# Performance work log

Hardware: AMD Instinct MI355X
Metric: run time of the kernel (lower is better)

The kernel has to match this reference:

```python
import jax, jax.numpy as jnp
import numpy as np

# Hardware-emulation constants (from init_kwargs, NeuroSim-style QLinear)
WL_IN = 8        # input activation bit width (bit-serial)
WL_W = 8         # weight bit width
CELL_BIT = 2     # bits per memory cell -> 4 weight slices
SUB = 128        # crossbar sub-array size (rows summed in analog)
ADC_BITS = 5     # ADC precision per partial sum
ONOFF = 10.0     # cell on/off conductance ratio
VARI = 0.05      # multiplicative device variation sigma


def _adc_quant(x, bits, axes):
    # LinearQuantizeOut: uniform quantization between tensor min/max
    mn = jnp.min(x, axis=axes, keepdims=True)
    mx = jnp.max(x, axis=axes, keepdims=True)
    step = (mx - mn) * (2.0 ** (-bits))
    step = jnp.where(step <= 0, 1.0, step)
    idx = jnp.clip(jnp.floor((x - mn) / step), 0.0, 2.0 ** bits - 1.0)
    return idx * step + mn


def _qlinear_hw(x, w, noise):
    """Analog PIM crossbar emulation of y = x @ w.T with bit-serial inputs,
    bit-sliced cells, on/off-ratio offset + dummy column, device variation,
    per-subarray ADC quantization."""
    B, N = x.shape
    F = w.shape[0]
    I, W, K = WL_IN, WL_W, WL_W // CELL_BIT
    cr = 2.0 ** CELL_BIT
    lower, upper = 1.0 / ONOFF, 1.0
    S = (N + SUB - 1) // SUB
    Np = S * SUB
    # quantize input to I bits in [0,1]; weight to W-bit integer in [0, 2^W-1]
    xq = jnp.round(jnp.clip(x, 0.0, 1.0) * (2.0 ** I - 1.0))            # [B, N]
    Xi = jnp.clip(jnp.round((w + 1.0) * 0.5 * (2.0 ** W - 1.0)), 0.0, 2.0 ** W - 1.0)  # [F, N]
    xq = jnp.pad(xq, ((0, 0), (0, Np - N)))
    Xi = jnp.pad(Xi, ((0, 0), (0, Np - N)))
    zpow = 2.0 ** jnp.arange(I, dtype=x.dtype)
    kpow = cr ** jnp.arange(K, dtype=x.dtype)
    bits = jnp.mod(jnp.floor(xq[..., None] / zpow), 2.0)                # [B, Np, I]
    slc = jnp.mod(jnp.floor(Xi[..., None] / kpow), cr)                  # [F, Np, K]
    g = slc * (upper - lower) + (cr - 1.0) * lower                      # cell conductances
    g = g * (1.0 + VARI * noise)                                        # device variation
    bits = bits.reshape(B, S, SUB, I)
    g = g.reshape(F, S, SUB, K)
    # analog partial sums per (input bit i, subarray s, weight slice k)
    P = jnp.einsum('bsai,fsak->iskbf', bits, g)                         # [I,S,K,B,F]
    # dummy column (all cells at lowest conductance), identical across F
    D = jnp.transpose(bits.sum(axis=2), (2, 1, 0)) * ((cr - 1.0) * lower)  # [I,S,B]
    Pq = _adc_quant(P, ADC_BITS, axes=(3, 4))
    Dq = _adc_quant(D, ADC_BITS, axes=(2,))
    scal = (2.0 ** jnp.arange(I, dtype=x.dtype))[:, None] * (cr ** jnp.arange(K, dtype=x.dtype))[None, :]
    acc = jnp.einsum('iskbf,ik->bf', Pq - Dq[:, :, None, :, None], scal) / (upper - lower)
    # undo integer mappings: w = 2*Xi/(2^W-1) - 1, x = xq/(2^I-1)
    out = 2.0 * acc / ((2.0 ** I - 1.0) * (2.0 ** W - 1.0)) \
          - xq.sum(axis=1, keepdims=True) / (2.0 ** I - 1.0)
    return out


def _qlinear(x, w, noise):
    # straight-through quantized weight (WAGE-style STE) + hardware forward
    Xi = jnp.clip(jnp.round((w + 1.0) * 0.5 * (2.0 ** WL_W - 1.0)), 0.0, 2.0 ** WL_W - 1.0)
    wq = 2.0 * Xi / (2.0 ** WL_W - 1.0) - 1.0
    wq_ste = w + jax.lax.stop_gradient(wq - w)
    out_ideal = x @ wq_ste.T
    out_hw = _qlinear_hw(x, w, noise)
    return out_ideal + jax.lax.stop_gradient(out_hw - out_ideal)


def setup_inputs() -> dict:
    key = jax.random.key(0)
    k1, k2, k3, k4, k5 = jax.random.split(key, 5)
    x = jax.random.uniform(k1, (1024, 784), dtype=jnp.float32)
    w1 = jax.random.normal(k2, (512, 784), dtype=jnp.float32) * 0.05
    w3 = jax.random.normal(k3, (10, 512), dtype=jnp.float32) * 0.08
    noise1 = jax.random.normal(k4, (512, 896, 4), dtype=jnp.float32)  # 784 padded to 7*128
    noise3 = jax.random.normal(k5, (10, 512, 4), dtype=jnp.float32)   # 512 = 4*128 exact
    return {"x": x, "w1": w1, "w3": w3, "noise1": noise1, "noise3": noise3}


def reference(x, w1, w3, noise1, noise3):
    h = jnp.tanh(_qlinear(x, w1, noise1))   # QLinear(784,512) + Tanh
    return _qlinear(h, w3, noise3)          # QLinear(512,10)
```

## Files before the change

### kernel.cpp

```cpp
#include <hip/hip_runtime.h>

#define FLTMAX 3.402823466e+38f


__global__ void init_kernel(float* __restrict__ acc1, unsigned* __restrict__ stats1)
{
    int gid = blockIdx.x * 256 + threadIdx.x;
    if (gid < 1024 * 512) acc1[gid] = 0.f;
    if (gid < 224) { stats1[gid * 2] = 0x7F7FFFFFu; stats1[gid * 2 + 1] = 0u; }
}

__global__ void prep1_kernel(const float* __restrict__ x, float* __restrict__ xq1,
                             float* __restrict__ sx1)
{
    __shared__ float red[128];
    int b = blockIdx.x;
    float psum = 0.f;
    for (int n = threadIdx.x; n < 896; n += 128) {
        float v = 0.f;
        if (n < 784) {
            float xv = x[b * 784 + n];
            xv = fminf(fmaxf(xv, 0.f), 1.f);
            v = rintf(__fmul_rn(xv, 255.f));
        }
        xq1[b * 896 + n] = v;
        psum += v;
    }
    red[threadIdx.x] = psum;
    __syncthreads();
    for (int w = 64; w >= 1; w >>= 1) {
        if (threadIdx.x < w) red[threadIdx.x] += red[threadIdx.x + w];
        __syncthreads();
    }
    if (threadIdx.x == 0) sx1[b] = red[0];
}

__global__ void prepg1_kernel(const float* __restrict__ w1, const float* __restrict__ noise1,
                              float* __restrict__ g1)
{
    int gid = blockIdx.x * 256 + threadIdx.x;
    if (gid >= 512 * 896) return;
    int f = gid / 896, n = gid % 896;
    float gv[4] = {0.f, 0.f, 0.f, 0.f};
    if (n < 784) {
        float w = w1[f * 784 + n];
        float Xi = fminf(fmaxf(rintf(__fmul_rn(__fmul_rn(__fadd_rn(w, 1.f), 0.5f), 255.f)),
                               0.f), 255.f);
        int xi = (int)Xi;
#pragma unroll
        for (int k = 0; k < 4; ++k) {
            int slc = (xi >> (2 * k)) & 3;
            float base = __fadd_rn(__fmul_rn((float)slc, 0.9f), 0.3f);
            float nf = __fadd_rn(1.f, __fmul_rn(0.05f, noise1[(f * 896 + n) * 4 + k]));
            gv[k] = __fmul_rn(base, nf);
        }
    }
#pragma unroll
    for (int k = 0; k < 4; ++k) g1[(k * 512 + f) * 896 + n] = gv[k];
}

__global__ void transpose_kernel(const float* __restrict__ in, float* __restrict__ out,
                                 int R, int C)
{
    __shared__ float tile[32][33];
    int c0 = blockIdx.x * 32, r0 = blockIdx.y * 32;
    int tx = threadIdx.x & 31, ty4 = (threadIdx.x >> 5) * 4;
#pragma unroll
    for (int u = 0; u < 4; ++u)
        tile[ty4 + u][tx] = in[(r0 + ty4 + u) * C + c0 + tx];
    __syncthreads();
#pragma unroll
    for (int u = 0; u < 4; ++u)
        out[(c0 + ty4 + u) * R + r0 + tx] = tile[tx][ty4 + u];
}

__global__ void prepg2_kernel(const float* __restrict__ w3, const float* __restrict__ noise3,
                              float* __restrict__ g2t)
{
    int gid = blockIdx.x * 256 + threadIdx.x;
    if (gid >= 10 * 512) return;
    int f = gid / 512, n = gid % 512;
    float w = w3[f * 512 + n];
    float Xi = fminf(fmaxf(rintf(__fmul_rn(__fmul_rn(__fadd_rn(w, 1.f), 0.5f), 255.f)),
                           0.f), 255.f);
    int xi = (int)Xi;
#pragma unroll
    for (int k = 0; k < 4; ++k) {
        int slc = (xi >> (2 * k)) & 3;
        float base = __fadd_rn(__fmul_rn((float)slc, 0.9f), 0.3f);
        float nf = __fadd_rn(1.f, __fmul_rn(0.05f, noise3[(f * 512 + n) * 4 + k]));
        g2t[n * 40 + k * 10 + f] = __fmul_rn(base, nf);
    }
}

__global__ void dq_kernel(const float* __restrict__ xq, float* __restrict__ Dq,
                          int S, int rowstride)
{
    __shared__ float red[512];
    const int i = blockIdx.x / S, s = blockIdx.x % S;
    const int tid = threadIdx.x;
    float D[4];
    float mn = FLTMAX, mx = -FLTMAX;
#pragma unroll
    for (int u = 0; u < 4; ++u) {
        int b = tid + u * 256;
        const float4* row = (const float4*)&xq[b * rowstride + s * 128];
        int c = 0;
#pragma unroll 8
        for (int q = 0; q < 32; ++q) {
            float4 v = row[q];
            c += (((int)v.x >> i) & 1) + (((int)v.y >> i) & 1) +
                 (((int)v.z >> i) & 1) + (((int)v.w >> i) & 1);
        }
        D[u] = __fmul_rn((float)c, 0.3f);
        mn = fminf(mn, D[u]);
        mx = fmaxf(mx, D[u]);
    }
    red[tid] = mn; red[256 + tid] = mx;
    __syncthreads();
    for (int w = 128; w >= 1; w >>= 1) {
        if (tid < w) {
            red[tid] = fminf(red[tid], red[tid + w]);
            red[256 + tid] = fmaxf(red[256 + tid], red[256 + tid + w]);
        }
        __syncthreads();
    }
    mn = red[0]; mx = red[256];
    float step = __fmul_rn(__fsub_rn(mx, mn), 0.03125f);
    if (step <= 0.f) step = 1.f;
#pragma unroll
    for (int u = 0; u < 4; ++u) {
        int b = tid + u * 256;
        float idx = fminf(fmaxf(floorf(__fdiv_rn(__fsub_rn(D[u], mn), step)), 0.f), 31.f);
        Dq[(i * S + s) * 1024 + b] = __fadd_rn(__fmul_rn(idx, step), mn);
    }
}

__global__ void dterm_kernel(const float* __restrict__ Dq, float* __restrict__ dterm, int S)
{
    int b = blockIdx.x * 256 + threadIdx.x;
    if (b >= 1024) return;
    float sum = 0.f;
    for (int i = 0; i < 8; ++i) {
        float sc = (float)(85 << i);
        for (int s = 0; s < S; ++s) sum = fmaf(Dq[(i * S + s) * 1024 + b], sc, sum);
    }
    dterm[b] = sum;
}

#define BK 32
__global__ __launch_bounds__(256, 4) void mm1_kernel(
    const float* __restrict__ xqT, const float* __restrict__ g1t,
    float* __restrict__ P, unsigned* __restrict__ stats, int s, int i0)
{
    __shared__ __align__(16) float As[BK][132];
    __shared__ __align__(16) float Bs[BK][132];
    __shared__ float red[512];
    const int tid = threadIdx.x;
    const int rowChunk = blockIdx.x * 128;
    const int i = i0 + (rowChunk >> 10);
    const int b0 = rowChunk & 1023;
    const int colBase = blockIdx.y * 128;
    const int nbase = s * 128;
    const int tx = tid & 15, ty = tid >> 4;

    float acc[8][8] = {};
    for (int ac = 0; ac < 4; ++ac) {
        const int n0 = nbase + ac * BK;
        __syncthreads();
#pragma unroll
        for (int u = 0; u < 4; ++u) {
            int t = u * 256 + tid;
            int a = t >> 5;
            int e = (t & 31) << 2;
            float4 av = *(const float4*)&xqT[(n0 + a) * 1024 + b0 + e];
            float4 bv = *(const float4*)&g1t[(n0 + a) * 2048 + colBase + e];
            float4 ab;
            ab.x = (float)((((int)av.x) >> i) & 1);
            ab.y = (float)((((int)av.y) >> i) & 1);
            ab.z = (float)((((int)av.z) >> i) & 1);
            ab.w = (float)((((int)av.w) >> i) & 1);
            *(float4*)&As[a][e] = ab;
            *(float4*)&Bs[a][e] = bv;
        }
        __syncthreads();
#pragma unroll 4
        for (int a = 0; a < BK; ++a) {
            float ar[8], br[8];
            *(float4*)&ar[0] = *(const float4*)&As[a][ty << 2];
            *(float4*)&ar[4] = *(const float4*)&As[a][64 + (ty << 2)];
            *(float4*)&br[0] = *(const float4*)&Bs[a][tx << 2];
            *(float4*)&br[4] = *(const float4*)&Bs[a][64 + (tx << 2)];
#pragma unroll
            for (int u = 0; u < 8; ++u)
#pragma unroll
                for (int v = 0; v < 8; ++v)
                    acc[u][v] = fmaf(ar[u], br[v], acc[u][v]);
        }
    }

#pragma unroll
    for (int uh = 0; uh < 2; ++uh)
#pragma unroll
        for (int u = 0; u < 4; ++u) {
            int row = rowChunk + uh * 64 + (ty << 2) + u;
#pragma unroll
            for (int vh = 0; vh < 2; ++vh) {
                float4 v = make_float4(acc[uh * 4 + u][vh * 4 + 0], acc[uh * 4 + u][vh * 4 + 1],
                                       acc[uh * 4 + u][vh * 4 + 2], acc[uh * 4 + u][vh * 4 + 3]);
                *(float4*)&P[(size_t)row * 2048 + colBase + vh * 64 + (tx << 2)] = v;
            }
        }

    float mn = acc[0][0], mx = acc[0][0];
#pragma unroll
    for (int u = 0; u < 8; ++u)
#pragma unroll
        for (int v = 0; v < 8; ++v) { mn = fminf(mn, acc[u][v]); mx = fmaxf(mx, acc[u][v]); }
    red[tid] = mn; red[256 + tid] = mx;
    __syncthreads();
    for (int w = 128; w >= 1; w >>= 1) {
        if (tid < w) {
            red[tid] = fminf(red[tid], red[tid + w]);
            red[256 + tid] = fmaxf(red[256 + tid], red[256 + tid + w]);
        }
        __syncthreads();
    }
    if (tid == 0) {
        int k = colBase >> 9;
        int slot = ((s * 8 + i) * 4 + k) * 2;
        atomicMin(&stats[slot], __float_as_uint(red[0]));
        atomicMax(&stats[slot + 1], __float_as_uint(red[256]));
    }
}

__global__ void quant1_kernel(const float* __restrict__ P, const unsigned* __restrict__ stats,
                              float* __restrict__ acc1, int s, int i0, int ni)
{
    int gid = blockIdx.x * 256 + threadIdx.x;
    int b = gid >> 9, f = gid & 511;
    float sum = 0.f;
    for (int il = 0; il < ni; ++il) {
        int i = i0 + il;
#pragma unroll
        for (int k = 0; k < 4; ++k) {
            int slot = ((s * 8 + i) * 4 + k) * 2;
            float mn = __uint_as_float(stats[slot]);
            float mx = __uint_as_float(stats[slot + 1]);
            float step = __fmul_rn(__fsub_rn(mx, mn), 0.03125f);
            if (step <= 0.f) step = 1.f;
            float val = P[(size_t)(il * 1024 + b) * 2048 + (k << 9) + f];
            float idx = fminf(fmaxf(floorf(__fdiv_rn(__fsub_rn(val, mn), step)), 0.f), 31.f);
            float pq = __fadd_rn(__fmul_rn(idx, step), mn);
            sum = fmaf(pq, (float)(1 << (i + 2 * k)), sum);
        }
    }
    acc1[gid] += sum;
}

__global__ void finish1_kernel(const float* __restrict__ acc1, const float* __restrict__ dterm1,
                               const float* __restrict__ sx1, float* __restrict__ xq2)
{
    int gid = blockIdx.x * 256 + threadIdx.x;
    int b = gid >> 9;
    float total = __fsub_rn(acc1[gid], dterm1[b]);
    float acc = __fdiv_rn(total, 0.9f);
    float o = __fsub_rn(__fdiv_rn(__fmul_rn(2.f, acc), 65025.f), __fdiv_rn(sx1[b], 255.f));
    float h = tanhf(o);
    h = fminf(fmaxf(h, 0.f), 1.f);
    xq2[gid] = rintf(__fmul_rn(h, 255.f));
}

__global__ void sx2_kernel(const float* __restrict__ xq2, float* __restrict__ sx2)
{
    __shared__ float red[128];
    int b = blockIdx.x;
    float psum = 0.f;
    for (int n = threadIdx.x; n < 512; n += 128) psum += xq2[b * 512 + n];
    red[threadIdx.x] = psum;
    __syncthreads();
    for (int w = 64; w >= 1; w >>= 1) {
        if (threadIdx.x < w) red[threadIdx.x] += red[threadIdx.x + w];
        __syncthreads();
    }
    if (threadIdx.x == 0) sx2[b] = red[0];
}

__global__ void mm2_kernel(const float* __restrict__ xq2, const float* __restrict__ g2t,
                           float* __restrict__ P2)
{
    int gid = blockIdx.x * 256 + threadIdx.x;
    if (gid >= 40960) return;
    int f = gid % 10;
    int b = (gid / 10) & 1023;
    int s = gid / 10240;
    float acc[8][4] = {};
    for (int a = 0; a < 128; ++a) {
        int n = s * 128 + a;
        int xi = (int)xq2[b * 512 + n];
        float g0 = g2t[n * 40 + f];
        float gA = g2t[n * 40 + 10 + f];
        float gB = g2t[n * 40 + 20 + f];
        float gC = g2t[n * 40 + 30 + f];
#pragma unroll
        for (int i = 0; i < 8; ++i) {
            float bi = (float)((xi >> i) & 1);
            acc[i][0] = fmaf(bi, g0, acc[i][0]);
            acc[i][1] = fmaf(bi, gA, acc[i][1]);
            acc[i][2] = fmaf(bi, gB, acc[i][2]);
            acc[i][3] = fmaf(bi, gC, acc[i][3]);
        }
    }
#pragma unroll
    for (int i = 0; i < 8; ++i)
#pragma unroll
        for (int k = 0; k < 4; ++k)
            P2[(size_t)((s * 8 + i) * 4 + k) * 10240 + b * 10 + f] = acc[i][k];
}

__global__ void stat2_kernel(const float* __restrict__ P2, float2* __restrict__ stats2)
{
    __shared__ float red[512];
    int p = blockIdx.x;
    int tid = threadIdx.x;
    float mn = FLTMAX, mx = -FLTMAX;
    for (int t = tid; t < 10240; t += 256) {
        float v = P2[(size_t)p * 10240 + t];
        mn = fminf(mn, v); mx = fmaxf(mx, v);
    }
    red[tid] = mn; red[256 + tid] = mx;
    __syncthreads();
    for (int w = 128; w >= 1; w >>= 1) {
        if (tid < w) {
            red[tid] = fminf(red[tid], red[tid + w]);
            red[256 + tid] = fmaxf(red[256 + tid], red[256 + tid + w]);
        }
        __syncthreads();
    }
    if (tid == 0) {
        float step = __fmul_rn(__fsub_rn(red[256], red[0]), 0.03125f);
        if (step <= 0.f) step = 1.f;
        stats2[p] = make_float2(red[0], step);
    }
}

__global__ void out2_kernel(const float* __restrict__ P2, const float2* __restrict__ stats2,
                            const float* __restrict__ dterm2, const float* __restrict__ sx2,
                            float* __restrict__ out)
{
    int gid = blockIdx.x * 256 + threadIdx.x;
    if (gid >= 10240) return;
    int b = gid / 10;
    float sum = 0.f;
    for (int s = 0; s < 4; ++s)
        for (int i = 0; i < 8; ++i)
#pragma unroll
            for (int k = 0; k < 4; ++k) {
                int p = (s * 8 + i) * 4 + k;
                float2 st = stats2[p];
                float val = P2[(size_t)p * 10240 + gid];
                float idx = fminf(fmaxf(floorf(__fdiv_rn(__fsub_rn(val, st.x), st.y)), 0.f), 31.f);
                float pq = __fadd_rn(__fmul_rn(idx, st.y), st.x);
                sum = fmaf(pq, (float)(1 << (i + 2 * k)), sum);
            }
    float total = __fsub_rn(sum, dterm2[b]);
    float acc = __fdiv_rn(total, 0.9f);
    out[gid] = __fsub_rn(__fdiv_rn(__fmul_rn(2.f, acc), 65025.f), __fdiv_rn(sx2[b], 255.f));
}

extern "C" void kernel_launch(void* const* d_in, const int* in_sizes, int n_in,
                              void* d_out, int out_size, void* d_ws, size_t ws_size,
                              hipStream_t stream)
{
    const float* x      = (const float*)d_in[0];
    const float* w1     = (const float*)d_in[1];
    const float* w3     = (const float*)d_in[2];
    const float* noise1 = (const float*)d_in[3];
    const float* noise3 = (const float*)d_in[4];
    float* out = (float*)d_out;
    float* ws  = (float*)d_ws;

    float*    xq1    = ws + 0;
    float*    g1     = ws + 917504;
    float*    acc1   = ws + 2752512;
    float*    xq2    = ws + 3276800;
    float*    P2     = ws + 3801088;
    float*    g2t    = ws + 5111808;
    float*    Dq1    = ws + 5132288;
    float*    Dq2    = ws + 5189632;
    float*    sx1    = ws + 5222400;
    float*    sx2    = ws + 5223424;
    float*    dterm1 = ws + 5224448;
    float*    dterm2 = ws + 5225472;
    float2*   stats2 = (float2*)(ws + 5226496);
    unsigned* stats1 = (unsigned*)(ws + 5226752);
    float*    xqT    = ws + 5227200;
    float*    g1t    = ws + 6144704;
    float*    Ps     = ws + 7979712;

    const size_t fixedf = 7979712;
    int ni = 8;
    while (ni > 1 && (fixedf + (size_t)ni * 2097152) * sizeof(float) > ws_size) ni >>= 1;

    init_kernel<<<2048, 256, 0, stream>>>(acc1, stats1);
    prep1_kernel<<<1024, 128, 0, stream>>>(x, xq1, sx1);
    prepg1_kernel<<<1792, 256, 0, stream>>>(w1, noise1, g1);
    transpose_kernel<<<dim3(28, 32), 256, 0, stream>>>(xq1, xqT, 1024, 896);
    transpose_kernel<<<dim3(28, 64), 256, 0, stream>>>(g1, g1t, 2048, 896);
    dq_kernel<<<56, 256, 0, stream>>>(xq1, Dq1, 7, 896);
    dterm_kernel<<<4, 256, 0, stream>>>(Dq1, dterm1, 7);

    for (int s = 0; s < 7; ++s)
        for (int i0 = 0; i0 < 8; i0 += ni) {
            mm1_kernel<<<dim3(8 * ni, 16), 256, 0, stream>>>(xqT, g1t, Ps, stats1, s, i0);
            quant1_kernel<<<2048, 256, 0, stream>>>(Ps, stats1, acc1, s, i0, ni);
        }

    finish1_kernel<<<2048, 256, 0, stream>>>(acc1, dterm1, sx1, xq2);
    sx2_kernel<<<1024, 128, 0, stream>>>(xq2, sx2);
    prepg2_kernel<<<20, 256, 0, stream>>>(w3, noise3, g2t);
    dq_kernel<<<32, 256, 0, stream>>>(xq2, Dq2, 4, 512);
    dterm_kernel<<<4, 256, 0, stream>>>(Dq2, dterm2, 4);
    mm2_kernel<<<160, 256, 0, stream>>>(xq2, g2t, P2);
    stat2_kernel<<<128, 256, 0, stream>>>(P2, stats2);
    out2_kernel<<<40, 256, 0, stream>>>(P2, stats2, dterm2, sx2, out);
}
```

Measured before the change: 683.6 us.

## Enlarge mm1 tile with register prefetch, vectorize quant, fuse g1 prep and transpose

```diff
diff --git a/kernel.cpp b/kernel.cpp
--- a/kernel.cpp
+++ b/kernel.cpp
@@ -35,28 +35,49 @@
     if (threadIdx.x == 0) sx1[b] = red[0];
 }
 
-__global__ void prepg1_kernel(const float* __restrict__ w1, const float* __restrict__ noise1,
-                              float* __restrict__ g1)
-{
-    int gid = blockIdx.x * 256 + threadIdx.x;
-    if (gid >= 512 * 896) return;
-    int f = gid / 896, n = gid % 896;
-    float gv[4] = {0.f, 0.f, 0.f, 0.f};
-    if (n < 784) {
-        float w = w1[f * 784 + n];
-        float Xi = fminf(fmaxf(rintf(__fmul_rn(__fmul_rn(__fadd_rn(w, 1.f), 0.5f), 255.f)),
-                               0.f), 255.f);
-        int xi = (int)Xi;
-#pragma unroll
-        for (int k = 0; k < 4; ++k) {
-            int slc = (xi >> (2 * k)) & 3;
-            float base = __fadd_rn(__fmul_rn((float)slc, 0.9f), 0.3f);
-            float nf = __fadd_rn(1.f, __fmul_rn(0.05f, noise1[(f * 896 + n) * 4 + k]));
-            gv[k] = __fmul_rn(base, nf);
-        }
-    }
-#pragma unroll
-    for (int k = 0; k < 4; ++k) g1[(k * 512 + f) * 896 + n] = gv[k];
+__global__ void prepg1t_kernel(const float* __restrict__ w1, const float* __restrict__ noise1,
+                               float* __restrict__ g1t)
+{
+    __shared__ float t[4][32][33];
+    const int n0 = blockIdx.x * 32, f0 = blockIdx.y * 32;
+    const int tid = threadIdx.x;
+    {
+        int n = tid & 31, fi = tid >> 5;
+#pragma unroll
+        for (int p = 0; p < 4; ++p) {
+            int f = p * 8 + fi;
+            int gn = n0 + n, gf = f0 + f;
+            float gv[4] = {0.f, 0.f, 0.f, 0.f};
+            if (gn < 784) {
+                float w = w1[gf * 784 + gn];
+                float Xi = fminf(fmaxf(rintf(__fmul_rn(__fmul_rn(__fadd_rn(w, 1.f), 0.5f), 255.f)),
+                                       0.f), 255.f);
+                int xi = (int)Xi;
+                float4 nz = *(const float4*)&noise1[(gf * 896 + gn) * 4];
+                float nzv[4] = {nz.x, nz.y, nz.z, nz.w};
+#pragma unroll
+                for (int k = 0; k < 4; ++k) {
+                    int slc = (xi >> (2 * k)) & 3;
+                    float base = __fadd_rn(__fmul_rn((float)slc, 0.9f), 0.3f);
+                    float nf = __fadd_rn(1.f, __fmul_rn(0.05f, nzv[k]));
+                    gv[k] = __fmul_rn(base, nf);
+                }
+            }
+#pragma unroll
+            for (int k = 0; k < 4; ++k) t[k][n][f] = gv[k];
+        }
+    }
+    __syncthreads();
+    {
+        int f = tid & 31, nn = tid >> 5;
+#pragma unroll
+        for (int p = 0; p < 4; ++p) {
+            int n = p * 8 + nn;
+#pragma unroll
+            for (int k = 0; k < 4; ++k)
+                g1t[(n0 + n) * 2048 + k * 512 + f0 + f] = t[k][n][f];
+        }
+    }
 }
 
 __global__ void transpose_kernel(const float* __restrict__ in, float* __restrict__ out,
@@ -149,50 +170,74 @@
 }
 
 #define BK 32
-__global__ __launch_bounds__(256, 4) void mm1_kernel(
+__global__ __launch_bounds__(256, 2) void mm1_kernel(
     const float* __restrict__ xqT, const float* __restrict__ g1t,
     float* __restrict__ P, unsigned* __restrict__ stats, int s, int i0)
 {
-    __shared__ __align__(16) float As[BK][132];
-    __shared__ __align__(16) float Bs[BK][132];
+    __shared__ __align__(16) float As[BK][256];
+    __shared__ __align__(16) float Bs[BK][128];
     __shared__ float red[512];
     const int tid = threadIdx.x;
-    const int rowChunk = blockIdx.x * 128;
-    const int i = i0 + (rowChunk >> 10);
-    const int b0 = rowChunk & 1023;
+    const int row0 = blockIdx.x * 256;
+    const int i = i0 + (row0 >> 10);
+    const int b0 = row0 & 1023;
     const int colBase = blockIdx.y * 128;
     const int nbase = s * 128;
     const int tx = tid & 15, ty = tid >> 4;
 
-    float acc[8][8] = {};
+    const int aA = tid >> 6;
+    const int eA = (tid & 63) << 2;
+    const int aB = tid >> 5;
+    const int eB = (tid & 31) << 2;
+
+    float4 pA[8], pB[4];
+#pragma unroll
+    for (int u = 0; u < 8; ++u)
+        pA[u] = *(const float4*)&xqT[(nbase + u * 4 + aA) * 1024 + b0 + eA];
+#pragma unroll
+    for (int u = 0; u < 4; ++u)
+        pB[u] = *(const float4*)&g1t[(nbase + u * 8 + aB) * 2048 + colBase + eB];
+
+    float acc[16][8] = {};
+
     for (int ac = 0; ac < 4; ++ac) {
-        const int n0 = nbase + ac * BK;
-        __syncthreads();
-#pragma unroll
-        for (int u = 0; u < 4; ++u) {
-            int t = u * 256 + tid;
-            int a = t >> 5;
-            int e = (t & 31) << 2;
-            float4 av = *(const float4*)&xqT[(n0 + a) * 1024 + b0 + e];
-            float4 bv = *(const float4*)&g1t[(n0 + a) * 2048 + colBase + e];
+        __syncthreads();
+#pragma unroll
+        for (int u = 0; u < 8; ++u) {
+            float4 av = pA[u];
             float4 ab;
             ab.x = (float)((((int)av.x) >> i) & 1);
             ab.y = (float)((((int)av.y) >> i) & 1);
             ab.z = (float)((((int)av.z) >> i) & 1);
             ab.w = (float)((((int)av.w) >> i) & 1);
-            *(float4*)&As[a][e] = ab;
-            *(float4*)&Bs[a][e] = bv;
-        }
-        __syncthreads();
-#pragma unroll 4
+            *(float4*)&As[u * 4 + aA][eA] = ab;
+        }
+#pragma unroll
+        for (int u = 0; u < 4; ++u)
+            *(float4*)&Bs[u * 8 + aB][eB] = pB[u];
+        __syncthreads();
+
+        if (ac < 3) {
+            const int n0 = nbase + (ac + 1) * BK;
+#pragma unroll
+            for (int u = 0; u < 8; ++u)
+                pA[u] = *(const float4*)&xqT[(n0 + u * 4 + aA) * 1024 + b0 + eA];
+#pragma unroll
+            for (int u = 0; u < 4; ++u)
+                pB[u] = *(const float4*)&g1t[(n0 + u * 8 + aB) * 2048 + colBase + eB];
+        }
+
+#pragma unroll 2
         for (int a = 0; a < BK; ++a) {
-            float ar[8], br[8];
-            *(float4*)&ar[0] = *(const float4*)&As[a][ty << 2];
-            *(float4*)&ar[4] = *(const float4*)&As[a][64 + (ty << 2)];
-            *(float4*)&br[0] = *(const float4*)&Bs[a][tx << 2];
-            *(float4*)&br[4] = *(const float4*)&Bs[a][64 + (tx << 2)];
-#pragma unroll
-            for (int u = 0; u < 8; ++u)
+            float ar[16], br[8];
+            *(float4*)&ar[0]  = *(const float4*)&As[a][(ty << 2)];
+            *(float4*)&ar[4]  = *(const float4*)&As[a][64 + (ty << 2)];
+            *(float4*)&ar[8]  = *(const float4*)&As[a][128 + (ty << 2)];
+            *(float4*)&ar[12] = *(const float4*)&As[a][192 + (ty << 2)];
+            *(float4*)&br[0]  = *(const float4*)&Bs[a][(tx << 2)];
+            *(float4*)&br[4]  = *(const float4*)&Bs[a][64 + (tx << 2)];
+#pragma unroll
+            for (int u = 0; u < 16; ++u)
 #pragma unroll
                 for (int v = 0; v < 8; ++v)
                     acc[u][v] = fmaf(ar[u], br[v], acc[u][v]);
@@ -200,21 +245,21 @@
     }
 
 #pragma unroll
-    for (int uh = 0; uh < 2; ++uh)
+    for (int q = 0; q < 4; ++q)
 #pragma unroll
         for (int u = 0; u < 4; ++u) {
-            int row = rowChunk + uh * 64 + (ty << 2) + u;
+            int row = row0 + q * 64 + (ty << 2) + u;
 #pragma unroll
             for (int vh = 0; vh < 2; ++vh) {
-                float4 v = make_float4(acc[uh * 4 + u][vh * 4 + 0], acc[uh * 4 + u][vh * 4 + 1],
-                                       acc[uh * 4 + u][vh * 4 + 2], acc[uh * 4 + u][vh * 4 + 3]);
+                float4 v = make_float4(acc[q * 4 + u][vh * 4 + 0], acc[q * 4 + u][vh * 4 + 1],
+                                       acc[q * 4 + u][vh * 4 + 2], acc[q * 4 + u][vh * 4 + 3]);
                 *(float4*)&P[(size_t)row * 2048 + colBase + vh * 64 + (tx << 2)] = v;
             }
         }
 
     float mn = acc[0][0], mx = acc[0][0];
 #pragma unroll
-    for (int u = 0; u < 8; ++u)
+    for (int u = 0; u < 16; ++u)
 #pragma unroll
         for (int v = 0; v < 8; ++v) { mn = fminf(mn, acc[u][v]); mx = fmaxf(mx, acc[u][v]); }
     red[tid] = mn; red[256 + tid] = mx;
@@ -238,8 +283,8 @@
                               float* __restrict__ acc1, int s, int i0, int ni)
 {
     int gid = blockIdx.x * 256 + threadIdx.x;
-    int b = gid >> 9, f = gid & 511;
-    float sum = 0.f;
+    int b = gid >> 7, f4 = gid & 127;
+    float4 sum = make_float4(0.f, 0.f, 0.f, 0.f);
     for (int il = 0; il < ni; ++il) {
         int i = i0 + il;
 #pragma unroll
@@ -249,13 +294,23 @@
             float mx = __uint_as_float(stats[slot + 1]);
             float step = __fmul_rn(__fsub_rn(mx, mn), 0.03125f);
             if (step <= 0.f) step = 1.f;
-            float val = P[(size_t)(il * 1024 + b) * 2048 + (k << 9) + f];
-            float idx = fminf(fmaxf(floorf(__fdiv_rn(__fsub_rn(val, mn), step)), 0.f), 31.f);
-            float pq = __fadd_rn(__fmul_rn(idx, step), mn);
-            sum = fmaf(pq, (float)(1 << (i + 2 * k)), sum);
-        }
-    }
-    acc1[gid] += sum;
+            float4 val = *(const float4*)&P[(size_t)(il * 1024 + b) * 2048 + (k << 9) + (f4 << 2)];
+            float sc = (float)(1 << (i + 2 * k));
+            float ix, pq;
+            ix = fminf(fmaxf(floorf(__fdiv_rn(__fsub_rn(val.x, mn), step)), 0.f), 31.f);
+            pq = __fadd_rn(__fmul_rn(ix, step), mn); sum.x = fmaf(pq, sc, sum.x);
+            ix = fminf(fmaxf(floorf(__fdiv_rn(__fsub_rn(val.y, mn), step)), 0.f), 31.f);
+            pq = __fadd_rn(__fmul_rn(ix, step), mn); sum.y = fmaf(pq, sc, sum.y);
+            ix = fminf(fmaxf(floorf(__fdiv_rn(__fsub_rn(val.z, mn), step)), 0.f), 31.f);
+            pq = __fadd_rn(__fmul_rn(ix, step), mn); sum.z = fmaf(pq, sc, sum.z);
+            ix = fminf(fmaxf(floorf(__fdiv_rn(__fsub_rn(val.w, mn), step)), 0.f), 31.f);
+            pq = __fadd_rn(__fmul_rn(ix, step), mn); sum.w = fmaf(pq, sc, sum.w);
+        }
+    }
+    float4* ap = (float4*)&acc1[(b << 9) + (f4 << 2)];
+    float4 a = *ap;
+    a.x += sum.x; a.y += sum.y; a.z += sum.z; a.w += sum.w;
+    *ap = a;
 }
 
 __global__ void finish1_kernel(const float* __restrict__ acc1, const float* __restrict__ dterm1,
@@ -381,7 +436,7 @@
     float* ws  = (float*)d_ws;
 
     float*    xq1    = ws + 0;
-    float*    g1     = ws + 917504;
+    float*    g1t    = ws + 917504;
     float*    acc1   = ws + 2752512;
     float*    xq2    = ws + 3276800;
     float*    P2     = ws + 3801088;
@@ -394,26 +449,24 @@
     float*    dterm2 = ws + 5225472;
     float2*   stats2 = (float2*)(ws + 5226496);
     unsigned* stats1 = (unsigned*)(ws + 5226752);
-    float*    xqT    = ws + 5227200;
-    float*    g1t    = ws + 6144704;
-    float*    Ps     = ws + 7979712;
-
-    const size_t fixedf = 7979712;
+    float*    xqT    = ws + 5227264;
+    float*    Ps     = ws + 6144768;
+
+    const size_t fixedf = 6144768;
     int ni = 8;
     while (ni > 1 && (fixedf + (size_t)ni * 2097152) * sizeof(float) > ws_size) ni >>= 1;
 
     init_kernel<<<2048, 256, 0, stream>>>(acc1, stats1);
     prep1_kernel<<<1024, 128, 0, stream>>>(x, xq1, sx1);
-    prepg1_kernel<<<1792, 256, 0, stream>>>(w1, noise1, g1);
+    prepg1t_kernel<<<dim3(28, 16), 256, 0, stream>>>(w1, noise1, g1t);
     transpose_kernel<<<dim3(28, 32), 256, 0, stream>>>(xq1, xqT, 1024, 896);
-    transpose_kernel<<<dim3(28, 64), 256, 0, stream>>>(g1, g1t, 2048, 896);
     dq_kernel<<<56, 256, 0, stream>>>(xq1, Dq1, 7, 896);
     dterm_kernel<<<4, 256, 0, stream>>>(Dq1, dterm1, 7);
 
     for (int s = 0; s < 7; ++s)
         for (int i0 = 0; i0 < 8; i0 += ni) {
-            mm1_kernel<<<dim3(8 * ni, 16), 256, 0, stream>>>(xqT, g1t, Ps, stats1, s, i0);
-            quant1_kernel<<<2048, 256, 0, stream>>>(Ps, stats1, acc1, s, i0, ni);
+            mm1_kernel<<<dim3(4 * ni, 16), 256, 0, stream>>>(xqT, g1t, Ps, stats1, s, i0);
+            quant1_kernel<<<512, 256, 0, stream>>>(Ps, stats1, acc1, s, i0, ni);
         }
 
     finish1_kernel<<<2048, 256, 0, stream>>>(acc1, dterm1, sx1, xq2);
```

Measured after the change: 704.0 us. 3.0% more time.
